# Kernel optimization log

Measured on AMD Instinct MI355X. Metric: run time of the kernel, lower is better.

The kernel has to match this reference:

```python
import jax, jax.numpy as jnp
import numpy as np

B = 65536
IN_F = 1024
OUT_F = 1024
N_ACT = 4  # len(activation_functions): tanh, sin, relu, sigmoid (cyclic over columns)


def setup_inputs() -> dict:
    key = jax.random.key(0)
    k1, k2 = jax.random.split(key)
    x = jax.random.normal(k1, (B, IN_F), dtype=jnp.float32)
    # xavier_uniform for weight [out, in]
    limit = float(np.sqrt(6.0 / (IN_F + OUT_F)))
    W = jax.random.uniform(k2, (OUT_F, IN_F), dtype=jnp.float32, minval=-limit, maxval=limit)
    b = jnp.zeros((OUT_F,), dtype=jnp.float32)
    return {"input": x, "W": W, "b": b}


def _apply_cyclic_acts(y):
    # column i gets activation (i % N_ACT); OUT_F % N_ACT == 0 so reshape to groups
    Bb, O = y.shape
    yg = y.reshape(Bb, O // N_ACT, N_ACT)
    out = jnp.stack([
        jnp.tanh(yg[..., 0]),
        jnp.sin(yg[..., 1]),
        jax.nn.relu(yg[..., 2]),
        jax.nn.sigmoid(yg[..., 3]),
    ], axis=-1)
    return out.reshape(Bb, O)


def reference(input, W, b) -> jnp.ndarray:
    y = jnp.einsum('bi,oi->bo', input, W) + b  # F.linear
    return _apply_cyclic_acts(y)
```

## Files before the change

### kernel.cpp

```cpp
#include <hip/hip_runtime.h>

constexpr int B_ROWS = 65536;
constexpr int IN_F   = 1024;
constexpr int OUT_F  = 1024;

constexpr int BDIM = 512;
constexpr int BM = 256, BN = 256, BK = 64;

typedef __bf16 bf16x8 __attribute__((ext_vector_type(8)));
typedef float  f32x4  __attribute__((ext_vector_type(4)));

__device__ __forceinline__ bf16x8 cvt8(f32x4 u0, f32x4 u1) {
    bf16x8 v;
    v[0] = (__bf16)u0[0]; v[1] = (__bf16)u0[1]; v[2] = (__bf16)u0[2]; v[3] = (__bf16)u0[3];
    v[4] = (__bf16)u1[0]; v[5] = (__bf16)u1[1]; v[6] = (__bf16)u1[2]; v[7] = (__bf16)u1[3];
    return v;
}

__device__ __forceinline__ void glds16(const __bf16* g, unsigned char* l) {
    __builtin_amdgcn_global_load_lds(
        (const __attribute__((address_space(1))) unsigned int*)(const void*)g,
        (__attribute__((address_space(3))) unsigned int*)(void*)l,
        16, 0, 0);
}

__global__ __launch_bounds__(256)
void cvt_all(const float* __restrict__ X, const float* __restrict__ W,
             __bf16* __restrict__ Xb, __bf16* __restrict__ Wb) {
    const int b = blockIdx.x;
    if (b < 2048) {
        size_t i = ((size_t)b * 256 + threadIdx.x) * 16;
        #pragma unroll 1
        for (int it = 0; it < 8; ++it, i += (size_t)2048 * 256 * 16) {
            f32x4 a0 = __builtin_nontemporal_load((const f32x4*)(X + i));
            f32x4 a1 = __builtin_nontemporal_load((const f32x4*)(X + i + 4));
            f32x4 a2 = __builtin_nontemporal_load((const f32x4*)(X + i + 8));
            f32x4 a3 = __builtin_nontemporal_load((const f32x4*)(X + i + 12));
            *(bf16x8*)(Xb + i)     = cvt8(a0, a1);
            *(bf16x8*)(Xb + i + 8) = cvt8(a2, a3);
        }
    } else {
        const size_t i = ((size_t)(b - 2048) * 256 + threadIdx.x) * 16;
        f32x4 a0 = __builtin_nontemporal_load((const f32x4*)(W + i));
        f32x4 a1 = __builtin_nontemporal_load((const f32x4*)(W + i + 4));
        f32x4 a2 = __builtin_nontemporal_load((const f32x4*)(W + i + 8));
        f32x4 a3 = __builtin_nontemporal_load((const f32x4*)(W + i + 12));
        *(bf16x8*)(Wb + i)     = cvt8(a0, a1);
        *(bf16x8*)(Wb + i + 8) = cvt8(a2, a3);
    }
}

__global__ __launch_bounds__(BDIM, 2)
void fused_linear_act(const __bf16* __restrict__ Xb,
                      const __bf16* __restrict__ Wb,
                      const float* __restrict__ bias,
                      float* __restrict__ O)
{
    __shared__ __attribute__((aligned(16))) unsigned char lds[2 * 65536];

    const int bx  = blockIdx.x;
    const int xcd = bx & 7;
    const int idx = bx >> 3;
    const int nt  = idx & 3;
    const int mt  = xcd + 8 * (idx >> 2);
    const int m0 = mt * BM;
    const int n0 = nt * BN;

    const int tid  = threadIdx.x;
    const int lane = tid & 63;
    const int wave = tid >> 6;
    const int wr2  = wave >> 2;
    const int w4   = wave & 3;
    const int lrow = lane & 15;
    const int quad = lane >> 4;

    const __bf16* agp = Xb + (size_t)(m0 + 32 * wave + lrow) * IN_F + quad * 8;
    const __bf16* bgp = Wb + (size_t)(n0 + 32 * wave + lrow) * IN_F + quad * 8;

    unsigned char* const b0 = lds;
    unsigned char* const b1 = lds + 65536;

    f32x4 acc[8][4];
    #pragma unroll
    for (int i = 0; i < 8; ++i)
        #pragma unroll
        for (int j = 0; j < 4; ++j)
            acc[i][j] = (f32x4){0.f, 0.f, 0.f, 0.f};

    bf16x8 aq0, aq1, aq2, aq3, bq0, bq1, bq2, bq3;

#define GA(BUF, KH, K) do { unsigned char* _d = (BUF) + (KH) * 16384 + wave * 2048; \
    glds16(agp + (K), _d); glds16(agp + (K) + 16 * IN_F, _d + 1024); } while (0)
#define GB(BUF, KH, K) do { unsigned char* _d = (BUF) + 32768 + (KH) * 16384 + wave * 2048; \
    glds16(bgp + (K), _d); glds16(bgp + (K) + 16 * IN_F, _d + 1024); } while (0)
#define RA(BUF, KH, MH) do { \
    const unsigned char* _r = (BUF) + (KH) * 16384 + (wr2 * 8 + (MH) * 4) * 1024 + lane * 16; \
    aq0 = *(const bf16x8*)(_r);        aq1 = *(const bf16x8*)(_r + 1024); \
    aq2 = *(const bf16x8*)(_r + 2048); aq3 = *(const bf16x8*)(_r + 3072); } while (0)
#define RB(BUF, KH) do { \
    const unsigned char* _r = (BUF) + 32768 + (KH) * 16384 + (w4 * 4) * 1024 + lane * 16; \
    bq0 = *(const bf16x8*)(_r);        bq1 = *(const bf16x8*)(_r + 1024); \
    bq2 = *(const bf16x8*)(_r + 2048); bq3 = *(const bf16x8*)(_r + 3072); } while (0)
#define MFMA1(MH, I, J) acc[(MH)*4+(I)][(J)] = \
    __builtin_amdgcn_mfma_f32_16x16x32_bf16(aq##I, bq##J, acc[(MH)*4+(I)][(J)], 0, 0, 0)
#define MFMAQ(MH) do { __builtin_amdgcn_s_setprio(1); \
    MFMA1(MH,0,0); MFMA1(MH,0,1); MFMA1(MH,0,2); MFMA1(MH,0,3); \
    MFMA1(MH,1,0); MFMA1(MH,1,1); MFMA1(MH,1,2); MFMA1(MH,1,3); \
    MFMA1(MH,2,0); MFMA1(MH,2,1); MFMA1(MH,2,2); MFMA1(MH,2,3); \
    MFMA1(MH,3,0); MFMA1(MH,3,1); MFMA1(MH,3,2); MFMA1(MH,3,3); \
    __builtin_amdgcn_s_setprio(0); } while (0)
#define BAR() __builtin_amdgcn_s_barrier()
#define VM4() asm volatile("s_waitcnt vmcnt(4)" ::: "memory")
#define VM0() asm volatile("s_waitcnt vmcnt(0)" ::: "memory")

#define SROUND(CUR, OPP, KT) do { \
    GA(OPP, 1, ((KT) + 1) * 64 + 32); RB(CUR, 0); RA(CUR, 0, 0); \
             BAR(); MFMAQ(0); BAR(); \
    GB(OPP, 1, ((KT) + 1) * 64 + 32); RA(CUR, 0, 1); \
             BAR(); MFMAQ(1); BAR(); \
    GA(CUR, 0, ((KT) + 2) * 64); RB(CUR, 1); RA(CUR, 1, 0); \
             BAR(); MFMAQ(0); BAR(); \
    GB(CUR, 0, ((KT) + 2) * 64); RA(CUR, 1, 1); \
             BAR(); MFMAQ(1); VM4(); BAR(); \
} while (0)

    GA(b0, 0, 0);  GB(b0, 0, 0);
    GA(b0, 1, 32); GB(b0, 1, 32);
    GA(b1, 0, 64); GB(b1, 0, 64);
    VM4();
    BAR();

    #pragma unroll 1
    for (int kt = 0; kt < 14; kt += 2) {
        SROUND(b0, b1, kt);
        SROUND(b1, b0, kt + 1);
    }
    GA(b1, 1, 15 * 64 + 32); RB(b0, 0); RA(b0, 0, 0); BAR(); MFMAQ(0); BAR();
    GB(b1, 1, 15 * 64 + 32); RA(b0, 0, 1);            BAR(); MFMAQ(1); BAR();
    RB(b0, 1); RA(b0, 1, 0);                          BAR(); MFMAQ(0); BAR();
    RA(b0, 1, 1);                                     BAR(); MFMAQ(1); VM0(); BAR();
    RB(b1, 0); RA(b1, 0, 0); BAR(); MFMAQ(0); BAR();
    RA(b1, 0, 1);            BAR(); MFMAQ(1); BAR();
    RB(b1, 1); RA(b1, 1, 0); BAR(); MFMAQ(0); BAR();
    RA(b1, 1, 1);            BAR(); MFMAQ(1);

    const int s = lane & 3;
    const float kmul = (s == 0) ? -2.f : -1.f;
    const float aa   = (s == 0) ?  2.f :  1.f;
    const float cc   = (s == 0) ? -1.f :  0.f;
    const bool  is_sin  = (s == 1);
    const bool  is_relu = (s == 2);

    float bv[4];
    #pragma unroll
    for (int fn = 0; fn < 4; ++fn) bv[fn] = bias[n0 + w4 * 64 + fn * 16 + lrow];

    #pragma unroll
    for (int fm = 0; fm < 8; ++fm) {
        #pragma unroll
        for (int r = 0; r < 4; ++r) {
            const int gr = m0 + wr2 * 128 + fm * 16 + quad * 4 + r;
            float* op = O + (size_t)gr * OUT_F + n0 + w4 * 64 + lrow;
            #pragma unroll
            for (int fn = 0; fn < 4; ++fn) {
                const float y = acc[fm][fn][r] + bv[fn];
                const float e = __expf(kmul * y);
                const float g = fmaf(aa, __builtin_amdgcn_rcpf(1.f + e), cc);
                const float sv = __sinf(y);
                const float rv = fmaxf(y, 0.f);
                const float res = is_sin ? sv : (is_relu ? rv : g);
                op[fn * 16] = res;
            }
        }
    }
}

__global__ __launch_bounds__(256)
void w_to_bf16(const float* __restrict__ W, __bf16* __restrict__ Wb) {
    const size_t i = ((size_t)blockIdx.x * 256 + threadIdx.x) * 16;
    f32x4 a0 = *(const f32x4*)(W + i);
    f32x4 a1 = *(const f32x4*)(W + i + 4);
    f32x4 a2 = *(const f32x4*)(W + i + 8);
    f32x4 a3 = *(const f32x4*)(W + i + 12);
    *(bf16x8*)(Wb + i)     = cvt8(a0, a1);
    *(bf16x8*)(Wb + i + 8) = cvt8(a2, a3);
}

__global__ __launch_bounds__(BDIM, 2)
void fused_fallback(const float* __restrict__ X, const __bf16* __restrict__ Wb,
                    const float* __restrict__ bias, float* __restrict__ O)
{
    __shared__ __attribute__((aligned(16))) unsigned char lds[2 * 65536];
    const int bx  = blockIdx.x;
    const int xcd = bx & 7;
    const int idx = bx >> 3;
    const int nt  = idx & 3;
    const int mt  = xcd + 8 * (idx >> 2);
    const int m0 = mt * BM;
    const int n0 = nt * BN;
    const int tid  = threadIdx.x;
    const int lane = tid & 63;
    const int wave = tid >> 6;
    const int wr2  = wave >> 2;
    const int w4   = wave & 3;
    const int lrow = lane & 15;
    const int quad = lane >> 4;
    const int arow = tid >> 1;
    const int ah   = tid & 1;
    const float* asrc = X + (size_t)(m0 + arow) * IN_F + ah * 32;
    const int awr = ah * 16384 + (arow >> 4) * 1024 + (arow & 15) * 16;
    const __bf16* bgp = Wb + (size_t)(n0 + 32 * wave + lrow) * IN_F + quad * 8;
    unsigned char* const b0 = lds;
    unsigned char* const b1 = lds + 65536;
    f32x4 acc[8][4];
    #pragma unroll
    for (int i = 0; i < 8; ++i)
        #pragma unroll
        for (int j = 0; j < 4; ++j)
            acc[i][j] = (f32x4){0.f, 0.f, 0.f, 0.f};
    f32x4 ar0, ar1, ar2, ar3, ar4, ar5, ar6, ar7;
    bf16x8 aq0, aq1, aq2, aq3, bq0, bq1, bq2, bq3;
#define ALOAD(KA) do { \
    ar0 = *(const f32x4*)(asrc + (KA));      ar1 = *(const f32x4*)(asrc + (KA) + 4);  \
    ar2 = *(const f32x4*)(asrc + (KA) + 8);  ar3 = *(const f32x4*)(asrc + (KA) + 12); \
    ar4 = *(const f32x4*)(asrc + (KA) + 16); ar5 = *(const f32x4*)(asrc + (KA) + 20); \
    ar6 = *(const f32x4*)(asrc + (KA) + 24); ar7 = *(const f32x4*)(asrc + (KA) + 28); } while (0)
#define DSW(BUF) do { unsigned char* _w = (BUF) + awr; \
    *(bf16x8*)(_w)       = cvt8(ar0, ar1); \
    *(bf16x8*)(_w + 256) = cvt8(ar2, ar3); \
    *(bf16x8*)(_w + 512) = cvt8(ar4, ar5); \
    *(bf16x8*)(_w + 768) = cvt8(ar6, ar7); } while (0)
#define GBALL(BUF, K) do { unsigned char* _d0 = (BUF) + 32768 + wave * 2048; \
    unsigned char* _d1 = _d0 + 16384; \
    glds16(bgp + (K), _d0);      glds16(bgp + (K) + 16 * IN_F, _d0 + 1024); \
    glds16(bgp + (K) + 32, _d1); glds16(bgp + (K) + 32 + 16 * IN_F, _d1 + 1024); } while (0)
#define FROUND(CUR, OPP, DO_STAGE, KB1, DO_ALOAD, KA2, VMW) do { \
    if (DO_STAGE) { GBALL(OPP, KB1); DSW(OPP); } \
    if (DO_ALOAD) { ALOAD(KA2); __builtin_amdgcn_sched_barrier(0); } \
    RB(CUR, 0); RA(CUR, 0, 0); BAR(); MFMAQ(0); BAR(); \
    RA(CUR, 0, 1); BAR(); MFMAQ(1); BAR(); \
    RB(CUR, 1); RA(CUR, 1, 0); BAR(); MFMAQ(0); BAR(); \
    RA(CUR, 1, 1); BAR(); MFMAQ(1); VMW; BAR(); \
} while (0)
    ALOAD(0);
    GBALL(b0, 0);
    DSW(b0);
    ALOAD(64);
    asm volatile("s_waitcnt vmcnt(8) lgkmcnt(0)" ::: "memory");
    BAR();
    #pragma unroll 1
    for (int t = 0; t < 14; t += 2) {
        FROUND(b0, b1, true, (t + 1) * 64, true, (t + 2) * 64, asm volatile("s_waitcnt vmcnt(8)" ::: "memory"));
        FROUND(b1, b0, true, (t + 2) * 64, true, (t + 3) * 64, asm volatile("s_waitcnt vmcnt(8)" ::: "memory"));
    }
    FROUND(b0, b1, true, 15 * 64, false, 0, VM0());
    FROUND(b1, b0, false, 0, false, 0, (void)0);
    const int s = lane & 3;
    const float kmul = (s == 0) ? -2.f : -1.f;
    const float aa   = (s == 0) ?  2.f :  1.f;
    const float cc   = (s == 0) ? -1.f :  0.f;
    const bool  is_sin  = (s == 1);
    const bool  is_relu = (s == 2);
    float bv[4];
    #pragma unroll
    for (int fn = 0; fn < 4; ++fn) bv[fn] = bias[n0 + w4 * 64 + fn * 16 + lrow];
    #pragma unroll
    for (int fm = 0; fm < 8; ++fm) {
        #pragma unroll
        for (int r = 0; r < 4; ++r) {
            const int gr = m0 + wr2 * 128 + fm * 16 + quad * 4 + r;
            float* op = O + (size_t)gr * OUT_F + n0 + w4 * 64 + lrow;
            #pragma unroll
            for (int fn = 0; fn < 4; ++fn) {
                const float y = acc[fm][fn][r] + bv[fn];
                const float e = __expf(kmul * y);
                const float gg = fmaf(aa, __builtin_amdgcn_rcpf(1.f + e), cc);
                const float sv = __sinf(y);
                const float rv = fmaxf(y, 0.f);
                const float res = is_sin ? sv : (is_relu ? rv : gg);
                op[fn * 16] = res;
            }
        }
    }
}

extern "C" void kernel_launch(void* const* d_in, const int* in_sizes, int n_in,
                              void* d_out, int out_size, void* d_ws, size_t ws_size,
                              hipStream_t stream) {
    const float* X = (const float*)d_in[0];
    const float* W = (const float*)d_in[1];
    const float* b = (const float*)d_in[2];
    float* O = (float*)d_out;

    const size_t nX = (size_t)B_ROWS * IN_F;
    const size_t nW = (size_t)OUT_F * IN_F;
    const int grid = (B_ROWS / BM) * (OUT_F / BN);

    if (ws_size >= (nW + nX) * sizeof(__bf16)) {
        __bf16* Wb = (__bf16*)d_ws;
        __bf16* Xb = (__bf16*)d_ws + nW;
        cvt_all<<<2048 + 256, 256, 0, stream>>>(X, W, Xb, Wb);
        fused_linear_act<<<grid, BDIM, 0, stream>>>(Xb, Wb, b, O);
    } else {
        __bf16* Wb = (__bf16*)d_ws;
        w_to_bf16<<<(int)(nW / (256 * 16)), 256, 0, stream>>>(W, Wb);
        fused_fallback<<<grid, BDIM, 0, stream>>>(X, Wb, b, O);
    }
}
```

Before: 596.0 us.

## Load B fragments directly to registers and triple-buffer A tiles in LDS

```diff
diff --git a/kernel.cpp b/kernel.cpp
--- a/kernel.cpp
+++ b/kernel.cpp
@@ -56,7 +56,7 @@
                       const float* __restrict__ bias,
                       float* __restrict__ O)
 {
-    __shared__ __attribute__((aligned(16))) unsigned char lds[2 * 65536];
+    __shared__ __attribute__((aligned(16))) unsigned char lds[3 * 32768];
 
     const int bx  = blockIdx.x;
     const int xcd = bx & 7;
@@ -75,10 +75,11 @@
     const int quad = lane >> 4;
 
     const __bf16* agp = Xb + (size_t)(m0 + 32 * wave + lrow) * IN_F + quad * 8;
-    const __bf16* bgp = Wb + (size_t)(n0 + 32 * wave + lrow) * IN_F + quad * 8;
+    const __bf16* bgp = Wb + (size_t)(n0 + w4 * 64 + lrow) * IN_F + quad * 8;
 
     unsigned char* const b0 = lds;
-    unsigned char* const b1 = lds + 65536;
+    unsigned char* const b1 = lds + 32768;
+    unsigned char* const b2 = lds + 65536;
 
     f32x4 acc[8][4];
     #pragma unroll
@@ -87,62 +88,82 @@
         for (int j = 0; j < 4; ++j)
             acc[i][j] = (f32x4){0.f, 0.f, 0.f, 0.f};
 
-    bf16x8 aq0, aq1, aq2, aq3, bq0, bq1, bq2, bq3;
-
-#define GA(BUF, KH, K) do { unsigned char* _d = (BUF) + (KH) * 16384 + wave * 2048; \
-    glds16(agp + (K), _d); glds16(agp + (K) + 16 * IN_F, _d + 1024); } while (0)
-#define GB(BUF, KH, K) do { unsigned char* _d = (BUF) + 32768 + (KH) * 16384 + wave * 2048; \
-    glds16(bgp + (K), _d); glds16(bgp + (K) + 16 * IN_F, _d + 1024); } while (0)
+    bf16x8 aq0, aq1, aq2, aq3;
+    bf16x8 bp0, bp1, bp2, bp3, bp4, bp5, bp6, bp7;
+    bf16x8 bq0, bq1, bq2, bq3, bq4, bq5, bq6, bq7;
+
+#define BLOAD(PFX, KT) do { const __bf16* _b = bgp + (size_t)(KT) * 64; \
+    PFX##0 = *(const bf16x8*)(_b);                PFX##1 = *(const bf16x8*)(_b + 16 * IN_F); \
+    PFX##2 = *(const bf16x8*)(_b + 32 * IN_F);    PFX##3 = *(const bf16x8*)(_b + 48 * IN_F); \
+    PFX##4 = *(const bf16x8*)(_b + 32);           PFX##5 = *(const bf16x8*)(_b + 32 + 16 * IN_F); \
+    PFX##6 = *(const bf16x8*)(_b + 32 + 32 * IN_F); PFX##7 = *(const bf16x8*)(_b + 32 + 48 * IN_F); \
+} while (0)
+#define GA4(STG, KT) do { unsigned char* _d = (STG) + wave * 2048; \
+    const __bf16* _a = agp + (size_t)(KT) * 64; \
+    glds16(_a, _d);            glds16(_a + 16 * IN_F, _d + 1024); \
+    glds16(_a + 32, _d + 16384); glds16(_a + 32 + 16 * IN_F, _d + 16384 + 1024); } while (0)
 #define RA(BUF, KH, MH) do { \
     const unsigned char* _r = (BUF) + (KH) * 16384 + (wr2 * 8 + (MH) * 4) * 1024 + lane * 16; \
     aq0 = *(const bf16x8*)(_r);        aq1 = *(const bf16x8*)(_r + 1024); \
     aq2 = *(const bf16x8*)(_r + 2048); aq3 = *(const bf16x8*)(_r + 3072); } while (0)
-#define RB(BUF, KH) do { \
-    const unsigned char* _r = (BUF) + 32768 + (KH) * 16384 + (w4 * 4) * 1024 + lane * 16; \
-    bq0 = *(const bf16x8*)(_r);        bq1 = *(const bf16x8*)(_r + 1024); \
-    bq2 = *(const bf16x8*)(_r + 2048); bq3 = *(const bf16x8*)(_r + 3072); } while (0)
-#define MFMA1(MH, I, J) acc[(MH)*4+(I)][(J)] = \
-    __builtin_amdgcn_mfma_f32_16x16x32_bf16(aq##I, bq##J, acc[(MH)*4+(I)][(J)], 0, 0, 0)
-#define MFMAQ(MH) do { __builtin_amdgcn_s_setprio(1); \
-    MFMA1(MH,0,0); MFMA1(MH,0,1); MFMA1(MH,0,2); MFMA1(MH,0,3); \
-    MFMA1(MH,1,0); MFMA1(MH,1,1); MFMA1(MH,1,2); MFMA1(MH,1,3); \
-    MFMA1(MH,2,0); MFMA1(MH,2,1); MFMA1(MH,2,2); MFMA1(MH,2,3); \
-    MFMA1(MH,3,0); MFMA1(MH,3,1); MFMA1(MH,3,2); MFMA1(MH,3,3); \
+#define MF16(MH, B0_, B1_, B2_, B3_) do { __builtin_amdgcn_s_setprio(1); \
+    acc[(MH)*4+0][0] = __builtin_amdgcn_mfma_f32_16x16x32_bf16(aq0, B0_, acc[(MH)*4+0][0], 0, 0, 0); \
+    acc[(MH)*4+0][1] = __builtin_amdgcn_mfma_f32_16x16x32_bf16(aq0, B1_, acc[(MH)*4+0][1], 0, 0, 0); \
+    acc[(MH)*4+0][2] = __builtin_amdgcn_mfma_f32_16x16x32_bf16(aq0, B2_, acc[(MH)*4+0][2], 0, 0, 0); \
+    acc[(MH)*4+0][3] = __builtin_amdgcn_mfma_f32_16x16x32_bf16(aq0, B3_, acc[(MH)*4+0][3], 0, 0, 0); \
+    acc[(MH)*4+1][0] = __builtin_amdgcn_mfma_f32_16x16x32_bf16(aq1, B0_, acc[(MH)*4+1][0], 0, 0, 0); \
+    acc[(MH)*4+1][1] = __builtin_amdgcn_mfma_f32_16x16x32_bf16(aq1, B1_, acc[(MH)*4+1][1], 0, 0, 0); \
+    acc[(MH)*4+1][2] = __builtin_amdgcn_mfma_f32_16x16x32_bf16(aq1, B2_, acc[(MH)*4+1][2], 0, 0, 0); \
+    acc[(MH)*4+1][3] = __builtin_amdgcn_mfma_f32_16x16x32_bf16(aq1, B3_, acc[(MH)*4+1][3], 0, 0, 0); \
+    acc[(MH)*4+2][0] = __builtin_amdgcn_mfma_f32_16x16x32_bf16(aq2, B0_, acc[(MH)*4+2][0], 0, 0, 0); \
+    acc[(MH)*4+2][1] = __builtin_amdgcn_mfma_f32_16x16x32_bf16(aq2, B1_, acc[(MH)*4+2][1], 0, 0, 0); \
+    acc[(MH)*4+2][2] = __builtin_amdgcn_mfma_f32_16x16x32_bf16(aq2, B2_, acc[(MH)*4+2][2], 0, 0, 0); \
+    acc[(MH)*4+2][3] = __builtin_amdgcn_mfma_f32_16x16x32_bf16(aq2, B3_, acc[(MH)*4+2][3], 0, 0, 0); \
+    acc[(MH)*4+3][0] = __builtin_amdgcn_mfma_f32_16x16x32_bf16(aq3, B0_, acc[(MH)*4+3][0], 0, 0, 0); \
+    acc[(MH)*4+3][1] = __builtin_amdgcn_mfma_f32_16x16x32_bf16(aq3, B1_, acc[(MH)*4+3][1], 0, 0, 0); \
+    acc[(MH)*4+3][2] = __builtin_amdgcn_mfma_f32_16x16x32_bf16(aq3, B2_, acc[(MH)*4+3][2], 0, 0, 0); \
+    acc[(MH)*4+3][3] = __builtin_amdgcn_mfma_f32_16x16x32_bf16(aq3, B3_, acc[(MH)*4+3][3], 0, 0, 0); \
     __builtin_amdgcn_s_setprio(0); } while (0)
 #define BAR() __builtin_amdgcn_s_barrier()
 #define VM4() asm volatile("s_waitcnt vmcnt(4)" ::: "memory")
 #define VM0() asm volatile("s_waitcnt vmcnt(0)" ::: "memory")
-
-#define SROUND(CUR, OPP, KT) do { \
-    GA(OPP, 1, ((KT) + 1) * 64 + 32); RB(CUR, 0); RA(CUR, 0, 0); \
-             BAR(); MFMAQ(0); BAR(); \
-    GB(OPP, 1, ((KT) + 1) * 64 + 32); RA(CUR, 0, 1); \
-             BAR(); MFMAQ(1); BAR(); \
-    GA(CUR, 0, ((KT) + 2) * 64); RB(CUR, 1); RA(CUR, 1, 0); \
-             BAR(); MFMAQ(0); BAR(); \
-    GB(CUR, 0, ((KT) + 2) * 64); RA(CUR, 1, 1); \
-             BAR(); MFMAQ(1); VM4(); BAR(); \
-} while (0)
-
-    GA(b0, 0, 0);  GB(b0, 0, 0);
-    GA(b0, 1, 32); GB(b0, 1, 32);
-    GA(b1, 0, 64); GB(b1, 0, 64);
-    VM4();
-    BAR();
+#define SB()  __builtin_amdgcn_sched_barrier(0)
+
+#define RND(CUR, STG, BU, BL, KTB, KTA) do { \
+    BLOAD(BL, KTB); SB(); \
+    GA4(STG, KTA);  SB(); \
+    RA(CUR, 0, 0); MF16(0, BU##0, BU##1, BU##2, BU##3); \
+    RA(CUR, 0, 1); MF16(1, BU##0, BU##1, BU##2, BU##3); \
+    RA(CUR, 1, 0); MF16(0, BU##4, BU##5, BU##6, BU##7); \
+    RA(CUR, 1, 1); MF16(1, BU##4, BU##5, BU##6, BU##7); \
+    VM4(); BAR(); } while (0)
+
+    GA4(b0, 0);
+    BLOAD(bp, 0); SB();
+    GA4(b1, 1);   SB();
+    VM4(); BAR();
 
     #pragma unroll 1
-    for (int kt = 0; kt < 14; kt += 2) {
-        SROUND(b0, b1, kt);
-        SROUND(b1, b0, kt + 1);
-    }
-    GA(b1, 1, 15 * 64 + 32); RB(b0, 0); RA(b0, 0, 0); BAR(); MFMAQ(0); BAR();
-    GB(b1, 1, 15 * 64 + 32); RA(b0, 0, 1);            BAR(); MFMAQ(1); BAR();
-    RB(b0, 1); RA(b0, 1, 0);                          BAR(); MFMAQ(0); BAR();
-    RA(b0, 1, 1);                                     BAR(); MFMAQ(1); VM0(); BAR();
-    RB(b1, 0); RA(b1, 0, 0); BAR(); MFMAQ(0); BAR();
-    RA(b1, 0, 1);            BAR(); MFMAQ(1); BAR();
-    RB(b1, 1); RA(b1, 1, 0); BAR(); MFMAQ(0); BAR();
-    RA(b1, 1, 1);            BAR(); MFMAQ(1);
+    for (int t6 = 0; t6 < 12; t6 += 6) {
+        RND(b0, b2, bp, bq, t6 + 1, t6 + 2);
+        RND(b1, b0, bq, bp, t6 + 2, t6 + 3);
+        RND(b2, b1, bp, bq, t6 + 3, t6 + 4);
+        RND(b0, b2, bq, bp, t6 + 4, t6 + 5);
+        RND(b1, b0, bp, bq, t6 + 5, t6 + 6);
+        RND(b2, b1, bq, bp, t6 + 6, t6 + 7);
+    }
+    RND(b0, b2, bp, bq, 13, 14);
+    RND(b1, b0, bq, bp, 14, 15);
+    BLOAD(bq, 15); SB();
+    RA(b2, 0, 0); MF16(0, bp0, bp1, bp2, bp3);
+    RA(b2, 0, 1); MF16(1, bp0, bp1, bp2, bp3);
+    RA(b2, 1, 0); MF16(0, bp4, bp5, bp6, bp7);
+    RA(b2, 1, 1); MF16(1, bp4, bp5, bp6, bp7);
+    VM0(); BAR();
+    RA(b0, 0, 0); MF16(0, bq0, bq1, bq2, bq3);
+    RA(b0, 0, 1); MF16(1, bq0, bq1, bq2, bq3);
+    RA(b0, 1, 0); MF16(0, bq4, bq5, bq6, bq7);
+    RA(b0, 1, 1); MF16(1, bq4, bq5, bq6, bq7);
 
     const int s = lane & 3;
     const float kmul = (s == 0) ? -2.f : -1.f;
@@ -190,7 +211,7 @@
 void fused_fallback(const float* __restrict__ X, const __bf16* __restrict__ Wb,
                     const float* __restrict__ bias, float* __restrict__ O)
 {
-    __shared__ __attribute__((aligned(16))) unsigned char lds[2 * 65536];
+    __shared__ __attribute__((aligned(16))) unsigned char lds[3 * 32768];
     const int bx  = blockIdx.x;
     const int xcd = bx & 7;
     const int idx = bx >> 3;
@@ -205,13 +226,16 @@
     const int w4   = wave & 3;
     const int lrow = lane & 15;
     const int quad = lane >> 4;
+
     const int arow = tid >> 1;
     const int ah   = tid & 1;
     const float* asrc = X + (size_t)(m0 + arow) * IN_F + ah * 32;
     const int awr = ah * 16384 + (arow >> 4) * 1024 + (arow & 15) * 16;
-    const __bf16* bgp = Wb + (size_t)(n0 + 32 * wave + lrow) * IN_F + quad * 8;
+    const __bf16* bgp = Wb + (size_t)(n0 + w4 * 64 + lrow) * IN_F + quad * 8;
+
     unsigned char* const b0 = lds;
-    unsigned char* const b1 = lds + 65536;
+    unsigned char* const b1 = lds + 32768;
+
     f32x4 acc[8][4];
     #pragma unroll
     for (int i = 0; i < 8; ++i)
@@ -219,42 +243,48 @@
         for (int j = 0; j < 4; ++j)
             acc[i][j] = (f32x4){0.f, 0.f, 0.f, 0.f};
     f32x4 ar0, ar1, ar2, ar3, ar4, ar5, ar6, ar7;
-    bf16x8 aq0, aq1, aq2, aq3, bq0, bq1, bq2, bq3;
-#define ALOAD(KA) do { \
+    bf16x8 aq0, aq1, aq2, aq3;
+    bf16x8 bp0, bp1, bp2, bp3, bp4, bp5, bp6, bp7;
+    bf16x8 bq0, bq1, bq2, bq3, bq4, bq5, bq6, bq7;
+
+#define ALOADF(KA) do { \
     ar0 = *(const f32x4*)(asrc + (KA));      ar1 = *(const f32x4*)(asrc + (KA) + 4);  \
     ar2 = *(const f32x4*)(asrc + (KA) + 8);  ar3 = *(const f32x4*)(asrc + (KA) + 12); \
     ar4 = *(const f32x4*)(asrc + (KA) + 16); ar5 = *(const f32x4*)(asrc + (KA) + 20); \
     ar6 = *(const f32x4*)(asrc + (KA) + 24); ar7 = *(const f32x4*)(asrc + (KA) + 28); } while (0)
-#define DSW(BUF) do { unsigned char* _w = (BUF) + awr; \
+#define DSWF(BUF) do { unsigned char* _w = (BUF) + awr; \
     *(bf16x8*)(_w)       = cvt8(ar0, ar1); \
     *(bf16x8*)(_w + 256) = cvt8(ar2, ar3); \
     *(bf16x8*)(_w + 512) = cvt8(ar4, ar5); \
     *(bf16x8*)(_w + 768) = cvt8(ar6, ar7); } while (0)
-#define GBALL(BUF, K) do { unsigned char* _d0 = (BUF) + 32768 + wave * 2048; \
-    unsigned char* _d1 = _d0 + 16384; \
-    glds16(bgp + (K), _d0);      glds16(bgp + (K) + 16 * IN_F, _d0 + 1024); \
-    glds16(bgp + (K) + 32, _d1); glds16(bgp + (K) + 32 + 16 * IN_F, _d1 + 1024); } while (0)
-#define FROUND(CUR, OPP, DO_STAGE, KB1, DO_ALOAD, KA2, VMW) do { \
-    if (DO_STAGE) { GBALL(OPP, KB1); DSW(OPP); } \
-    if (DO_ALOAD) { ALOAD(KA2); __builtin_amdgcn_sched_barrier(0); } \
-    RB(CUR, 0); RA(CUR, 0, 0); BAR(); MFMAQ(0); BAR(); \
-    RA(CUR, 0, 1); BAR(); MFMAQ(1); BAR(); \
-    RB(CUR, 1); RA(CUR, 1, 0); BAR(); MFMAQ(0); BAR(); \
-    RA(CUR, 1, 1); BAR(); MFMAQ(1); VMW; BAR(); \
-} while (0)
-    ALOAD(0);
-    GBALL(b0, 0);
-    DSW(b0);
-    ALOAD(64);
-    asm volatile("s_waitcnt vmcnt(8) lgkmcnt(0)" ::: "memory");
+#define FRND(CUR, OPP, BU, BL, KTB, KTA) do { \
+    BLOAD(BL, KTB); SB(); \
+    DSWF(OPP); \
+    if ((KTA) < 16 * 64) { ALOADF(KTA); SB(); } \
+    RA(CUR, 0, 0); MF16(0, BU##0, BU##1, BU##2, BU##3); \
+    RA(CUR, 0, 1); MF16(1, BU##0, BU##1, BU##2, BU##3); \
+    RA(CUR, 1, 0); MF16(0, BU##4, BU##5, BU##6, BU##7); \
+    RA(CUR, 1, 1); MF16(1, BU##4, BU##5, BU##6, BU##7); \
+    asm volatile("s_waitcnt lgkmcnt(0)" ::: "memory"); BAR(); } while (0)
+
+    ALOADF(0);
+    BLOAD(bp, 0); SB();
+    DSWF(b0);
+    ALOADF(64);
+    asm volatile("s_waitcnt lgkmcnt(0)" ::: "memory");
     BAR();
+
     #pragma unroll 1
     for (int t = 0; t < 14; t += 2) {
-        FROUND(b0, b1, true, (t + 1) * 64, true, (t + 2) * 64, asm volatile("s_waitcnt vmcnt(8)" ::: "memory"));
-        FROUND(b1, b0, true, (t + 2) * 64, true, (t + 3) * 64, asm volatile("s_waitcnt vmcnt(8)" ::: "memory"));
-    }
-    FROUND(b0, b1, true, 15 * 64, false, 0, VM0());
-    FROUND(b1, b0, false, 0, false, 0, (void)0);
+        FRND(b0, b1, bp, bq, t + 1, (t + 2) * 64);
+        FRND(b1, b0, bq, bp, t + 2, (t + 3) * 64);
+    }
+    FRND(b0, b1, bp, bq, 15, 16 * 64);
+    RA(b1, 0, 0); MF16(0, bq0, bq1, bq2, bq3);
+    RA(b1, 0, 1); MF16(1, bq0, bq1, bq2, bq3);
+    RA(b1, 1, 0); MF16(0, bq4, bq5, bq6, bq7);
+    RA(b1, 1, 1); MF16(1, bq4, bq5, bq6, bq7);
+
     const int s = lane & 3;
     const float kmul = (s == 0) ? -2.f : -1.f;
     const float aa   = (s == 0) ?  2.f :  1.f;
```

Result: slower. 656.1 us (+10.1%).
